# Kernel optimization log

Hardware: AMD Instinct MI355X
Metric: run time of the kernel (lower is better)

Reference implementation:

```python
import jax, jax.numpy as jnp
import numpy as np

B, D, H, L, T = 4096, 256, 512, 2, 45


def _lstm_cell(x, h, c, W_ih, W_hh, b_ih, b_hh):
    # PyTorch LSTM gate order: i, f, g, o
    gates = x @ W_ih + h @ W_hh + b_ih + b_hh  # [B, 4H]
    i, f, g, o = jnp.split(gates, 4, axis=-1)
    i = jax.nn.sigmoid(i)
    f = jax.nn.sigmoid(f)
    g = jnp.tanh(g)
    o = jax.nn.sigmoid(o)
    c_new = f * c + i * g
    h_new = o * jnp.tanh(c_new)
    return h_new, c_new


def setup_inputs() -> dict:
    key = jax.random.key(0)
    ks = jax.random.split(key, 32)
    s = 0.02
    inp = {
        "encoder_feat": jax.random.normal(ks[0], (B, D), jnp.float32),
        "context": jax.random.normal(ks[1], (B, D), jnp.float32),
        "initial_intent": jax.random.uniform(ks[2], (B, 1), jnp.float32),
        # hidden/cell init linears: d_model -> H*L (stored [in, out])
        "Wh_init": jax.random.normal(ks[3], (D, H * L), jnp.float32) * s,
        "bh_init": jnp.zeros((H * L,), jnp.float32),
        "Wc_init": jax.random.normal(ks[4], (D, H * L), jnp.float32) * s,
        "bc_init": jnp.zeros((H * L,), jnp.float32),
        # LSTM layer 0: input size 1 + d_model
        "W_ih0": jax.random.normal(ks[5], (1 + D, 4 * H), jnp.float32) * s,
        "W_hh0": jax.random.normal(ks[6], (H, 4 * H), jnp.float32) * s,
        "b_ih0": jnp.zeros((4 * H,), jnp.float32),
        "b_hh0": jnp.zeros((4 * H,), jnp.float32),
        # LSTM layer 1: input size H
        "W_ih1": jax.random.normal(ks[7], (H, 4 * H), jnp.float32) * s,
        "W_hh1": jax.random.normal(ks[8], (H, 4 * H), jnp.float32) * s,
        "b_ih1": jnp.zeros((4 * H,), jnp.float32),
        "b_hh1": jnp.zeros((4 * H,), jnp.float32),
        # output_proj: H -> 32 -> 1
        "Wo1": jax.random.normal(ks[9], (H, 32), jnp.float32) * s,
        "bo1": jnp.zeros((32,), jnp.float32),
        "Wo2": jax.random.normal(ks[10], (32, 1), jnp.float32) * s,
        "bo2": jnp.zeros((1,), jnp.float32),
        # global_intent_head: H -> 32 -> 1
        "Wg1": jax.random.normal(ks[11], (H, 32), jnp.float32) * s,
        "bg1": jnp.zeros((32,), jnp.float32),
        "Wg2": jax.random.normal(ks[12], (32, 1), jnp.float32) * s,
        "bg2": jnp.zeros((1,), jnp.float32),
    }
    return inp


def reference(encoder_feat, context, initial_intent,
              Wh_init, bh_init, Wc_init, bc_init,
              W_ih0, W_hh0, b_ih0, b_hh0,
              W_ih1, W_hh1, b_ih1, b_hh1,
              Wo1, bo1, Wo2, bo2, Wg1, bg1, Wg2, bg2):
    # init hidden/cell: [B, L*H] -> [B, L, H]; layer-major slices
    h_init = (encoder_feat @ Wh_init + bh_init).reshape(B, L, H)
    c_init = (encoder_feat @ Wc_init + bc_init).reshape(B, L, H)
    h0, h1 = h_init[:, 0], h_init[:, 1]
    c0, c1 = c_init[:, 0], c_init[:, 1]

    def step(carry, _):
        h0, c0, h1, c1, intent = carry
        x = jnp.concatenate([intent, context], axis=-1)  # [B, 1+D]
        h0n, c0n = _lstm_cell(x, h0, c0, W_ih0, W_hh0, b_ih0, b_hh0)
        h1n, c1n = _lstm_cell(h0n, h1, c1, W_ih1, W_hh1, b_ih1, b_hh1)
        logit = jax.nn.relu(h1n @ Wo1 + bo1) @ Wo2 + bo2  # [B, 1]
        intent_new = jax.nn.sigmoid(logit)
        return (h0n, c0n, h1n, c1n, intent_new), intent_new

    carry0 = (h0, c0, h1, c1, initial_intent)
    (h0, c0, h1, c1, _), ys = jax.lax.scan(step, carry0, None, length=T)
    step_intents = jnp.transpose(ys, (1, 0, 2))  # [B, T, 1]
    global_logit = jax.nn.relu(h1 @ Wg1 + bg1) @ Wg2 + bg2
    global_intent = jax.nn.sigmoid(global_logit)  # [B, 1]
    return step_intents, global_intent
```

## Files before the change

kernel.cpp:

```cpp
#include <hip/hip_runtime.h>
#include <hip/hip_bf16.h>

#define Bsz 4096
#define Dsz 256
#define Hsz 512
#define Tsz 45

typedef __attribute__((ext_vector_type(8))) short short8;
typedef __attribute__((ext_vector_type(4))) float f32x4;
typedef __attribute__((ext_vector_type(4))) unsigned short us4;
using bf16 = __hip_bfloat16;
using u8 = unsigned char;

__device__ __forceinline__ float sigf(float x)   { return 1.0f / (1.0f + __expf(-x)); }
__device__ __forceinline__ float tanhft(float x) { return 1.0f - 2.0f / (__expf(2.0f * x) + 1.0f); }
__device__ __forceinline__ float b2f(unsigned short u) { return __uint_as_float((unsigned)u << 16); }
__device__ __forceinline__ u8 f2fp8(float v) {
    int p = __builtin_amdgcn_cvt_pk_fp8_f32(v, v, 0, false);
    return (u8)(p & 0xff);
}

__device__ __forceinline__ void gload16(const void* g, void* l) {
    __builtin_amdgcn_global_load_lds((const __attribute__((address_space(1))) void*)g,
                                     (__attribute__((address_space(3))) void*)l, 16, 0, 0);
}

#define WAIT_VM(N) asm volatile("s_waitcnt vmcnt(" #N ")" ::: "memory")
#define WAIT_LGKM0 asm volatile("s_waitcnt lgkmcnt(0)" ::: "memory")

__global__ void k_conv(const float* __restrict__ ef,   const float* __restrict__ ctx,
                       const float* __restrict__ Whi,  const float* __restrict__ Wci,
                       const float* __restrict__ Wih0, const float* __restrict__ Whh0,
                       const float* __restrict__ Wih1, const float* __restrict__ Whh1,
                       const float* __restrict__ Wo1,  const float* __restrict__ Wg1,
                       bf16* __restrict__ efb,  bf16* __restrict__ ctxb,
                       bf16* __restrict__ Wit,  u8* __restrict__ W0p,
                       u8* __restrict__ W1p,  u8* __restrict__ Wo1p,
                       u8* __restrict__ Wg1p)
{
    size_t tid = (size_t)blockIdx.x * blockDim.x + threadIdx.x;
    size_t gsz = (size_t)gridDim.x * blockDim.x;
    for (size_t i = tid; i < (size_t)Bsz * Dsz; i += gsz) {
        efb[i]  = __float2bfloat16(ef[i]);
        ctxb[i] = __float2bfloat16(ctx[i]);
    }
    for (size_t i = tid; i < 2048ull * 512 / 4; i += gsz) {
        int n = i >> 7, k = (i & 127) * 4;
        int lo = __builtin_amdgcn_cvt_pk_fp8_f32(Whh0[(size_t)(k+0)*2048+n], Whh0[(size_t)(k+1)*2048+n], 0, false);
        int pk = __builtin_amdgcn_cvt_pk_fp8_f32(Whh0[(size_t)(k+2)*2048+n], Whh0[(size_t)(k+3)*2048+n], lo, true);
        int nb = n >> 4;
        size_t blk = (size_t)((k >> 5) * 8 + ((nb >> 2) & 7)) * 16 + ((nb >> 5) * 4 + (nb & 3));
        *(int*)(W0p + blk * 512 + ((k >> 3) & 3) * 128 + (n & 15) * 8 + (k & 4)) = pk;
    }
    for (size_t i = tid; i < 2048ull * 1024 / 4; i += gsz) {
        int n = i >> 8, k = (i & 255) * 4;
        float f0, f1, f2, f3;
        if (k < 512) {
            f0 = Wih1[(size_t)(k+0)*2048+n]; f1 = Wih1[(size_t)(k+1)*2048+n];
            f2 = Wih1[(size_t)(k+2)*2048+n]; f3 = Wih1[(size_t)(k+3)*2048+n];
        } else {
            int kk = k - 512;
            f0 = Whh1[(size_t)(kk+0)*2048+n]; f1 = Whh1[(size_t)(kk+1)*2048+n];
            f2 = Whh1[(size_t)(kk+2)*2048+n]; f3 = Whh1[(size_t)(kk+3)*2048+n];
        }
        int lo = __builtin_amdgcn_cvt_pk_fp8_f32(f0, f1, 0, false);
        int pk = __builtin_amdgcn_cvt_pk_fp8_f32(f2, f3, lo, true);
        int nb = n >> 4;
        size_t blk = (size_t)((k >> 5) * 8 + ((nb >> 2) & 7)) * 16 + ((nb >> 5) * 4 + (nb & 3));
        *(int*)(W1p + blk * 512 + ((k >> 3) & 3) * 128 + (n & 15) * 8 + (k & 4)) = pk;
    }
    for (size_t i = tid; i < 32ull * 512 / 4; i += gsz) {
        int n = i >> 7, k = (i & 127) * 4;
        size_t dst = ((size_t)(n >> 4) * 16 + (k >> 5)) * 512 + ((k >> 3) & 3) * 128 + (n & 15) * 8 + (k & 4);
        int lo = __builtin_amdgcn_cvt_pk_fp8_f32(Wo1[(size_t)(k+0)*32+n], Wo1[(size_t)(k+1)*32+n], 0, false);
        int pk = __builtin_amdgcn_cvt_pk_fp8_f32(Wo1[(size_t)(k+2)*32+n], Wo1[(size_t)(k+3)*32+n], lo, true);
        *(int*)(Wo1p + dst) = pk;
        lo = __builtin_amdgcn_cvt_pk_fp8_f32(Wg1[(size_t)(k+0)*32+n], Wg1[(size_t)(k+1)*32+n], 0, false);
        pk = __builtin_amdgcn_cvt_pk_fp8_f32(Wg1[(size_t)(k+2)*32+n], Wg1[(size_t)(k+3)*32+n], lo, true);
        *(int*)(Wg1p + dst) = pk;
    }
    for (size_t i = tid; i < 4096ull * 256; i += gsz) {
        size_t n = i >> 8, k = i & 255;
        float v = (n < 1024) ? Whi[k * 1024 + n]
                : (n < 2048) ? Wci[k * 1024 + (n - 1024)]
                             : Wih0[(1 + k) * 2048 + (n - 2048)];
        Wit[i] = __float2bfloat16(v);
    }
}

__global__ void __launch_bounds__(256)
k_init(const bf16* __restrict__ efb, const bf16* __restrict__ ctxb,
       const bf16* __restrict__ Wit,
       const float* __restrict__ bh,  const float* __restrict__ bc,
       const float* __restrict__ bi0, const float* __restrict__ bh0,
       u8* __restrict__ h0, u8* __restrict__ h1,
       float* __restrict__ c0, float* __restrict__ c1,
       bf16* __restrict__ ctxg)
{
    const int t = threadIdx.x, lane = t & 63, w = t >> 6;
    const int wr = w >> 1, wc = w & 1;
    const int lq = lane >> 4, ln = lane & 15;
    const int m0 = blockIdx.x * 128, n0 = blockIdx.y * 64;
    const bf16* A = (n0 < 2048) ? efb : ctxb;

    f32x4 zero = {0.f, 0.f, 0.f, 0.f};
    f32x4 acc[4][2];
#pragma unroll
    for (int r = 0; r < 4; ++r)
#pragma unroll
        for (int c = 0; c < 2; ++c) acc[r][c] = zero;

    for (int k0 = 0; k0 < 256; k0 += 32) {
        short8 af[4];
#pragma unroll
        for (int r = 0; r < 4; ++r)
            af[r] = *(const short8*)(A + (size_t)(m0 + wr * 64 + r * 16 + ln) * 256 + k0 + lq * 8);
#pragma unroll
        for (int c = 0; c < 2; ++c) {
            short8 bv = *(const short8*)(Wit + (size_t)(n0 + wc * 32 + c * 16 + ln) * 256 + k0 + lq * 8);
#pragma unroll
            for (int r = 0; r < 4; ++r)
                acc[r][c] = __builtin_amdgcn_mfma_f32_16x16x32_bf16(af[r], bv, acc[r][c], 0, 0, 0);
        }
    }
#pragma unroll
    for (int r = 0; r < 4; ++r)
#pragma unroll
        for (int c = 0; c < 2; ++c)
#pragma unroll
            for (int e = 0; e < 4; ++e) {
                int b = m0 + wr * 64 + r * 16 + lq * 4 + e;
                int n = n0 + wc * 32 + c * 16 + ln;
                float v = acc[r][c][e];
                if (n < 1024) {
                    v += bh[n];
                    if (n < 512) h0[(size_t)b * 512 + n]       = f2fp8(v);
                    else         h1[(size_t)b * 512 + n - 512] = f2fp8(v);
                } else if (n < 2048) {
                    int m = n - 1024; v += bc[m];
                    if (m < 512) c0[(size_t)b * 512 + m]       = v;
                    else         c1[(size_t)b * 512 + m - 512] = v;
                } else {
                    int j = n - 2048;
                    ctxg[(size_t)b * 2048 + (j & 511) * 4 + (j >> 9)] =
                        __float2bfloat16(v + bi0[j] + bh0[j]);
                }
            }
}

__device__ __forceinline__ long hread(const u8* buf, int ln, int lq, int kt) {
    int c = (kt << 2) + lq;
    return *(const long*)(buf + ln * 512 + ((c ^ ln) << 3));
}

__device__ __forceinline__ void stageW(const u8* __restrict__ Wp, int w, int kt,
                                       u8* slot, int lane) {
    const u8* src = Wp + ((size_t)(kt * 8 + w) << 13) + lane * 16;
#pragma unroll
    for (int i = 0; i < 8; ++i)
        gload16(src + i * 1024, slot + i * 1024);
}

__global__ void __launch_bounds__(512, 1)
k_loop(const u8* __restrict__ h0i, const u8* __restrict__ h1i,
       const u8* __restrict__ W0p, const u8* __restrict__ W1p,
       const u8* __restrict__ Wo1p, const u8* __restrict__ Wg1p,
       const bf16* __restrict__ ctxg, const float* __restrict__ ii,
       const float* __restrict__ w0row,
       const float* __restrict__ bi1, const float* __restrict__ bh1,
       const float* __restrict__ bo1, const float* __restrict__ Wo2,
       const float* __restrict__ bo2,
       const float* __restrict__ bg1, const float* __restrict__ Wg2,
       const float* __restrict__ bg2,
       const float* __restrict__ c0g, const float* __restrict__ c1g,
       float* __restrict__ out)
{
    __shared__ u8 h0L[8192];
    __shared__ u8 h1L[8192];
    __shared__ u8 Wring[8][2][8192];
    __shared__ float sit[16];
    __shared__ float spart[16][2];

    const int t = threadIdx.x, lane = t & 63, w = t >> 6;
    const int ln = lane & 15, lq = lane >> 4;
    const int m0 = blockIdx.x * 16;
    const int b = m0 + ln;
    f32x4 zero = {0.f, 0.f, 0.f, 0.f};

#pragma unroll
    for (int i = 0; i < 2; ++i) {
        int cid = i * 512 + t;
        int row = cid >> 6, c = cid & 63;
        long v0 = *(const long*)(h0i + (size_t)(m0 + row) * 512 + c * 8);
        long v1 = *(const long*)(h1i + (size_t)(m0 + row) * 512 + c * 8);
        int pc = row * 512 + ((c ^ row) << 3);
        *(long*)(&h0L[pc]) = v0;
        *(long*)(&h1L[pc]) = v1;
    }
    f32x4 cr0[4], cr1[4];
#pragma unroll
    for (int jc = 0; jc < 4; ++jc) {
        int jlb = (w * 4 + jc) * 16 + lq * 4;
        cr0[jc] = *(const f32x4*)(c0g + (size_t)b * 512 + jlb);
        cr1[jc] = *(const f32x4*)(c1g + (size_t)b * 512 + jlb);
    }
    __syncthreads();

    auto head2 = [&](const u8* Wp, const float* b1, const float* W2, float b2s,
                     bool tosit, float* dst, int stride, int scol) {
        if (w < 2) {
            f32x4 acc = zero;
#pragma unroll
            for (int kt = 0; kt < 16; ++kt) {
                long bf = hread(h1L, ln, lq, kt);
                long af = *(const long*)(Wp + (size_t)(w * 16 + kt) * 512 + lane * 8);
                acc = __builtin_amdgcn_mfma_f32_16x16x32_fp8_fp8(af, bf, acc, 0, 0, 0);
            }
            float v = 0.f;
#pragma unroll
            for (int e = 0; e < 4; ++e) {
                int j = w * 16 + lq * 4 + e;
                v += fmaxf(acc[e] + b1[j], 0.f) * W2[j];
            }
            v += __shfl_xor(v, 16);
            v += __shfl_xor(v, 32);
            if (lq == 0) spart[ln][w] = v;
        }
        __syncthreads();
        if (t < 16) {
            float pv = sigf(spart[t][0] + spart[t][1] + b2s);
            if (tosit) sit[t] = pv;
            if (dst) dst[(size_t)(m0 + t) * stride + scol] = pv;
        }
        __syncthreads();
    };

    for (int s = 0; s < Tsz; ++s) {
        if (s == 0) {
            if (t < 16) sit[t] = ii[m0 + t];
            __syncthreads();
        } else {
            head2(Wo1p, bo1, Wo2, bo2[0], true, out, Tsz, s - 1);
        }
        const float sval = sit[ln];

        {
            f32x4 acc[4][4];
#pragma unroll
            for (int jc = 0; jc < 4; ++jc)
#pragma unroll
                for (int g = 0; g < 4; ++g) acc[jc][g] = zero;

            WAIT_VM(0);
            stageW(W0p, w, 0, Wring[w][0], lane);
            stageW(W0p, w, 1, Wring[w][1], lane);
#pragma unroll 2
            for (int kt = 0; kt < 16; ++kt) {
                if (kt < 15) { WAIT_VM(8); } else { WAIT_VM(0); }
                long bf = hread(h0L, ln, lq, kt);
                const u8* slot = Wring[w][kt & 1];
#pragma unroll
                for (int q = 0; q < 16; ++q) {
                    long af = *(const long*)(slot + q * 512 + lane * 8);
                    acc[q & 3][q >> 2] = __builtin_amdgcn_mfma_f32_16x16x32_fp8_fp8(
                        af, bf, acc[q & 3][q >> 2], 0, 0, 0);
                }
                if (kt + 2 < 16) {
                    WAIT_LGKM0;
                    stageW(W0p, w, kt + 2, Wring[w][kt & 1], lane);
                }
            }
            int hold[4];
#pragma unroll
            for (int jc = 0; jc < 4; ++jc) {
                int jlb = (w * 4 + jc) * 16 + lq * 4;
                f32x4 a0v[4];
#pragma unroll
                for (int g = 0; g < 4; ++g) a0v[g] = *(const f32x4*)(w0row + g * 512 + jlb);
                float hv[4];
#pragma unroll
                for (int e = 0; e < 4; ++e) {
                    us4 xgv = *(const us4*)((const unsigned short*)ctxg + (size_t)b * 2048 + (jlb + e) * 4);
                    float pre[4];
#pragma unroll
                    for (int g = 0; g < 4; ++g)
                        pre[g] = acc[jc][g][e] + b2f(xgv[g]) + sval * a0v[g][e];
                    float ig = sigf(pre[0]), fg = sigf(pre[1]);
                    float gg = tanhft(pre[2]), og = sigf(pre[3]);
                    float cn = fg * cr0[jc][e] + ig * gg;
                    cr0[jc][e] = cn;
                    hv[e] = og * tanhft(cn);
                }
                int lo = __builtin_amdgcn_cvt_pk_fp8_f32(hv[0], hv[1], 0, false);
                hold[jc] = __builtin_amdgcn_cvt_pk_fp8_f32(hv[2], hv[3], lo, true);
            }
            __syncthreads();
#pragma unroll
            for (int jc = 0; jc < 4; ++jc) {
                int c = (w * 4 + jc) * 2 + (lq >> 1);
                *(int*)(h0L + ln * 512 + ((c ^ ln) << 3) + (lq & 1) * 4) = hold[jc];
            }
            WAIT_LGKM0;
            __syncthreads();
        }

        {
            f32x4 acc[4][4];
#pragma unroll
            for (int jc = 0; jc < 4; ++jc)
#pragma unroll
                for (int g = 0; g < 4; ++g) acc[jc][g] = zero;

            WAIT_VM(0);
            stageW(W1p, w, 0, Wring[w][0], lane);
            stageW(W1p, w, 1, Wring[w][1], lane);
#pragma unroll 2
            for (int kt = 0; kt < 32; ++kt) {
                if (kt < 31) { WAIT_VM(8); } else { WAIT_VM(0); }
                long bf = (kt < 16) ? hread(h0L, ln, lq, kt) : hread(h1L, ln, lq, kt - 16);
                const u8* slot = Wring[w][kt & 1];
#pragma unroll
                for (int q = 0; q < 16; ++q) {
                    long af = *(const long*)(slot + q * 512 + lane * 8);
                    acc[q & 3][q >> 2] = __builtin_amdgcn_mfma_f32_16x16x32_fp8_fp8(
                        af, bf, acc[q & 3][q >> 2], 0, 0, 0);
                }
                if (kt + 2 < 32) {
                    WAIT_LGKM0;
                    stageW(W1p, w, kt + 2, Wring[w][kt & 1], lane);
                }
            }
            int hold[4];
#pragma unroll
            for (int jc = 0; jc < 4; ++jc) {
                int jlb = (w * 4 + jc) * 16 + lq * 4;
                f32x4 a1v[4];
#pragma unroll
                for (int g = 0; g < 4; ++g) {
                    f32x4 bv1 = *(const f32x4*)(bi1 + g * 512 + jlb);
                    f32x4 bv2 = *(const f32x4*)(bh1 + g * 512 + jlb);
#pragma unroll
                    for (int e = 0; e < 4; ++e) a1v[g][e] = bv1[e] + bv2[e];
                }
                float hv[4];
#pragma unroll
                for (int e = 0; e < 4; ++e) {
                    float pre[4];
#pragma unroll
                    for (int g = 0; g < 4; ++g) pre[g] = acc[jc][g][e] + a1v[g][e];
                    float ig = sigf(pre[0]), fg = sigf(pre[1]);
                    float gg = tanhft(pre[2]), og = sigf(pre[3]);
                    float cn = fg * cr1[jc][e] + ig * gg;
                    cr1[jc][e] = cn;
                    hv[e] = og * tanhft(cn);
                }
                int lo = __builtin_amdgcn_cvt_pk_fp8_f32(hv[0], hv[1], 0, false);
                hold[jc] = __builtin_amdgcn_cvt_pk_fp8_f32(hv[2], hv[3], lo, true);
            }
            __syncthreads();
#pragma unroll
            for (int jc = 0; jc < 4; ++jc) {
                int c = (w * 4 + jc) * 2 + (lq >> 1);
                *(int*)(h1L + ln * 512 + ((c ^ ln) << 3) + (lq & 1) * 4) = hold[jc];
            }
            WAIT_LGKM0;
            __syncthreads();
        }
    }

    head2(Wo1p, bo1, Wo2, bo2[0], false, out, Tsz, 44);
    head2(Wg1p, bg1, Wg2, bg2[0], false, out + (size_t)Bsz * Tsz, 1, 0);
}

extern "C" void kernel_launch(void* const* d_in, const int* in_sizes, int n_in,
                              void* d_out, int out_size, void* d_ws, size_t ws_size,
                              hipStream_t stream)
{
    const float* ef   = (const float*)d_in[0];
    const float* ctx  = (const float*)d_in[1];
    const float* ii   = (const float*)d_in[2];
    const float* Whi  = (const float*)d_in[3];
    const float* bh   = (const float*)d_in[4];
    const float* Wci  = (const float*)d_in[5];
    const float* bc   = (const float*)d_in[6];
    const float* Wih0 = (const float*)d_in[7];
    const float* Whh0 = (const float*)d_in[8];
    const float* bi0  = (const float*)d_in[9];
    const float* bh0  = (const float*)d_in[10];
    const float* Wih1 = (const float*)d_in[11];
    const float* Whh1 = (const float*)d_in[12];
    const float* bi1  = (const float*)d_in[13];
    const float* bh1  = (const float*)d_in[14];
    const float* Wo1  = (const float*)d_in[15];
    const float* bo1  = (const float*)d_in[16];
    const float* Wo2  = (const float*)d_in[17];
    const float* bo2  = (const float*)d_in[18];
    const float* Wg1  = (const float*)d_in[19];
    const float* bg1  = (const float*)d_in[20];
    const float* Wg2  = (const float*)d_in[21];
    const float* bg2  = (const float*)d_in[22];
    float* out = (float*)d_out;

    char* ws = (char*)d_ws;
    size_t off = 0;
    auto take = [&](size_t bytes) -> char* {
        char* pp = ws + off;
        off += (bytes + 255) & ~(size_t)255;
        return pp;
    };
    u8*  W0p     = (u8*)take(2048ull * 512);
    u8*  W1p     = (u8*)take(2048ull * 1024);
    u8*  Wo1p    = (u8*)take(32ull * 512);
    u8*  Wg1p    = (u8*)take(32ull * 512);
    bf16* Wit    = (bf16*)take(4096ull * 256 * 2);
    bf16* efb    = (bf16*)take((size_t)Bsz * Dsz * 2);
    bf16* ctxb   = (bf16*)take((size_t)Bsz * Dsz * 2);
    u8*  h0x     = (u8*)take((size_t)Bsz * Hsz);
    u8*  h1x     = (u8*)take((size_t)Bsz * Hsz);
    float* c0    = (float*)take((size_t)Bsz * Hsz * 4);
    float* c1    = (float*)take((size_t)Bsz * Hsz * 4);
    bf16* ctxg   = (bf16*)take((size_t)Bsz * 2048 * 2);
    (void)ws_size; (void)in_sizes; (void)n_in; (void)out_size;

    k_conv<<<2048, 256, 0, stream>>>(ef, ctx, Whi, Wci, Wih0, Whh0, Wih1, Whh1, Wo1, Wg1,
                                     efb, ctxb, Wit, W0p, W1p, Wo1p, Wg1p);
    k_init<<<dim3(32, 64), 256, 0, stream>>>(efb, ctxb, Wit, bh, bc, bi0, bh0,
                                             h0x, h1x, c0, c1, ctxg);
    k_loop<<<256, 512, 0, stream>>>(h0x, h1x, W0p, W1p, Wo1p, Wg1p,
                                    ctxg, ii, Wih0, bi1, bh1,
                                    bo1, Wo2, bo2, bg1, Wg2, bg2,
                                    c0, c1, out);
}
```

Before: 2.681 ms.

## Deepen weight staging pipeline to four half-tile LDS slots

New measurement: 2.595 ms. 3.2% less time.

```diff
diff --git a/kernel.cpp b/kernel.cpp
--- a/kernel.cpp
+++ b/kernel.cpp
@@ -26,7 +26,6 @@
 }
 
 #define WAIT_VM(N) asm volatile("s_waitcnt vmcnt(" #N ")" ::: "memory")
-#define WAIT_LGKM0 asm volatile("s_waitcnt lgkmcnt(0)" ::: "memory")
 
 __global__ void k_conv(const float* __restrict__ ef,   const float* __restrict__ ctx,
                        const float* __restrict__ Whi,  const float* __restrict__ Wci,
@@ -153,12 +152,24 @@
     return *(const long*)(buf + ln * 512 + ((c ^ ln) << 3));
 }
 
-__device__ __forceinline__ void stageW(const u8* __restrict__ Wp, int w, int kt,
-                                       u8* slot, int lane) {
-    const u8* src = Wp + ((size_t)(kt * 8 + w) << 13) + lane * 16;
-#pragma unroll
-    for (int i = 0; i < 8; ++i)
-        gload16(src + i * 1024, slot + i * 1024);
+__device__ __forceinline__ void stageH(const u8* __restrict__ Wp, int w, int h,
+                                       u8* Wr, int lane) {
+    const u8* src = Wp + ((size_t)((h >> 1) * 8 + w) << 13) + ((size_t)(h & 1) << 12) + lane * 16;
+    u8* dst = Wr + ((size_t)(h & 3) << 12);
+#pragma unroll
+    for (int i = 0; i < 4; ++i)
+        gload16(src + i * 1024, dst + i * 1024);
+}
+
+template <int QB>
+__device__ __forceinline__ void mfma_half(const u8* slot, int lane, long bf,
+                                          f32x4 (&acc)[4][4]) {
+#pragma unroll
+    for (int i = 0; i < 8; ++i) {
+        long af = *(const long*)(slot + i * 512 + lane * 8);
+        acc[(QB + i) & 3][(QB + i) >> 2] =
+            __builtin_amdgcn_mfma_f32_16x16x32_fp8_fp8(af, bf, acc[(QB + i) & 3][(QB + i) >> 2], 0, 0, 0);
+    }
 }
 
 __global__ void __launch_bounds__(512, 1)
@@ -177,7 +188,7 @@
 {
     __shared__ u8 h0L[8192];
     __shared__ u8 h1L[8192];
-    __shared__ u8 Wring[8][2][8192];
+    __shared__ u8 WringS[8][16384];
     __shared__ float sit[16];
     __shared__ float spart[16][2];
 
@@ -185,6 +196,7 @@
     const int ln = lane & 15, lq = lane >> 4;
     const int m0 = blockIdx.x * 16;
     const int b = m0 + ln;
+    u8* Wr = WringS[w];
     f32x4 zero = {0.f, 0.f, 0.f, 0.f};
 
 #pragma unroll
@@ -252,23 +264,33 @@
                 for (int g = 0; g < 4; ++g) acc[jc][g] = zero;
 
             WAIT_VM(0);
-            stageW(W0p, w, 0, Wring[w][0], lane);
-            stageW(W0p, w, 1, Wring[w][1], lane);
+            stageH(W0p, w, 0, Wr, lane);
+            stageH(W0p, w, 1, Wr, lane);
+            stageH(W0p, w, 2, Wr, lane);
 #pragma unroll 2
-            for (int kt = 0; kt < 16; ++kt) {
-                if (kt < 15) { WAIT_VM(8); } else { WAIT_VM(0); }
+            for (int kt = 0; kt < 14; ++kt) {
                 long bf = hread(h0L, ln, lq, kt);
-                const u8* slot = Wring[w][kt & 1];
-#pragma unroll
-                for (int q = 0; q < 16; ++q) {
-                    long af = *(const long*)(slot + q * 512 + lane * 8);
-                    acc[q & 3][q >> 2] = __builtin_amdgcn_mfma_f32_16x16x32_fp8_fp8(
-                        af, bf, acc[q & 3][q >> 2], 0, 0, 0);
-                }
-                if (kt + 2 < 16) {
-                    WAIT_LGKM0;
-                    stageW(W0p, w, kt + 2, Wring[w][kt & 1], lane);
-                }
+                WAIT_VM(8);
+                mfma_half<0>(Wr + (size_t)((2 * kt) & 3) * 4096, lane, bf, acc);
+                stageH(W0p, w, 2 * kt + 3, Wr, lane);
+                WAIT_VM(8);
+                mfma_half<8>(Wr + (size_t)((2 * kt + 1) & 3) * 4096, lane, bf, acc);
+                stageH(W0p, w, 2 * kt + 4, Wr, lane);
+            }
+            {
+                long bf = hread(h0L, ln, lq, 14);
+                WAIT_VM(8);
+                mfma_half<0>(Wr + (size_t)(28 & 3) * 4096, lane, bf, acc);
+                stageH(W0p, w, 31, Wr, lane);
+                WAIT_VM(8);
+                mfma_half<8>(Wr + (size_t)(29 & 3) * 4096, lane, bf, acc);
+            }
+            {
+                long bf = hread(h0L, ln, lq, 15);
+                WAIT_VM(4);
+                mfma_half<0>(Wr + (size_t)(30 & 3) * 4096, lane, bf, acc);
+                WAIT_VM(0);
+                mfma_half<8>(Wr + (size_t)(31 & 3) * 4096, lane, bf, acc);
             }
             int hold[4];
 #pragma unroll
@@ -300,7 +322,7 @@
                 int c = (w * 4 + jc) * 2 + (lq >> 1);
                 *(int*)(h0L + ln * 512 + ((c ^ ln) << 3) + (lq & 1) * 4) = hold[jc];
             }
-            WAIT_LGKM0;
+            asm volatile("s_waitcnt lgkmcnt(0)" ::: "memory");
             __syncthreads();
         }
 
@@ -312,23 +334,43 @@
                 for (int g = 0; g < 4; ++g) acc[jc][g] = zero;
 
             WAIT_VM(0);
-            stageW(W1p, w, 0, Wring[w][0], lane);
-            stageW(W1p, w, 1, Wring[w][1], lane);
+            stageH(W1p, w, 0, Wr, lane);
+            stageH(W1p, w, 1, Wr, lane);
+            stageH(W1p, w, 2, Wr, lane);
 #pragma unroll 2
-            for (int kt = 0; kt < 32; ++kt) {
-                if (kt < 31) { WAIT_VM(8); } else { WAIT_VM(0); }
-                long bf = (kt < 16) ? hread(h0L, ln, lq, kt) : hread(h1L, ln, lq, kt - 16);
-                const u8* slot = Wring[w][kt & 1];
-#pragma unroll
-                for (int q = 0; q < 16; ++q) {
-                    long af = *(const long*)(slot + q * 512 + lane * 8);
-                    acc[q & 3][q >> 2] = __builtin_amdgcn_mfma_f32_16x16x32_fp8_fp8(
-                        af, bf, acc[q & 3][q >> 2], 0, 0, 0);
-                }
-                if (kt + 2 < 32) {
-                    WAIT_LGKM0;
-                    stageW(W1p, w, kt + 2, Wring[w][kt & 1], lane);
-                }
+            for (int kt = 0; kt < 16; ++kt) {
+                long bf = hread(h0L, ln, lq, kt);
+                WAIT_VM(8);
+                mfma_half<0>(Wr + (size_t)((2 * kt) & 3) * 4096, lane, bf, acc);
+                stageH(W1p, w, 2 * kt + 3, Wr, lane);
+                WAIT_VM(8);
+                mfma_half<8>(Wr + (size_t)((2 * kt + 1) & 3) * 4096, lane, bf, acc);
+                stageH(W1p, w, 2 * kt + 4, Wr, lane);
+            }
+#pragma unroll 2
+            for (int kt = 16; kt < 30; ++kt) {
+                long bf = hread(h1L, ln, lq, kt - 16);
+                WAIT_VM(8);
+                mfma_half<0>(Wr + (size_t)((2 * kt) & 3) * 4096, lane, bf, acc);
+                stageH(W1p, w, 2 * kt + 3, Wr, lane);
+                WAIT_VM(8);
+                mfma_half<8>(Wr + (size_t)((2 * kt + 1) & 3) * 4096, lane, bf, acc);
+                stageH(W1p, w, 2 * kt + 4, Wr, lane);
+            }
+            {
+                long bf = hread(h1L, ln, lq, 14);
+                WAIT_VM(8);
+                mfma_half<0>(Wr + (size_t)(60 & 3) * 4096, lane, bf, acc);
+                stageH(W1p, w, 63, Wr, lane);
+                WAIT_VM(8);
+                mfma_half<8>(Wr + (size_t)(61 & 3) * 4096, lane, bf, acc);
+            }
+            {
+                long bf = hread(h1L, ln, lq, 15);
+                WAIT_VM(4);
+                mfma_half<0>(Wr + (size_t)(62 & 3) * 4096, lane, bf, acc);
+                WAIT_VM(0);
+                mfma_half<8>(Wr + (size_t)(63 & 3) * 4096, lane, bf, acc);
             }
             int hold[4];
 #pragma unroll
@@ -363,7 +405,7 @@
                 int c = (w * 4 + jc) * 2 + (lq >> 1);
                 *(int*)(h1L + ln * 512 + ((c ^ ln) << 3) + (lq & 1) * 4) = hold[jc];
             }
-            WAIT_LGKM0;
+            asm volatile("s_waitcnt lgkmcnt(0)" ::: "memory");
             __syncthreads();
         }
     }
```
